# Kernel optimization log

Hardware: AMD Instinct MI355X
Metric: run time of the kernel (lower is better)

## Reference

```python
import jax, jax.numpy as jnp
import numpy as np

K = 1024          # num_embeddings
D = 64            # embedding_dim
EPS = 0.05        # entropic regularization epsilon
DUAL_STEPS = 10
DUAL_LR = 0.5
TEMP = 0.5        # hist_temperature
OT_W = 1.0
CC = 0.25         # commitment cost


def _norm_prob(p):
    p = jnp.clip(p, 1e-12)
    return p / p.sum()


def _dual_obj(phi, src_w, tgt_w, cost):
    src_w = _norm_prob(src_w)
    tgt_w = _norm_prob(tgt_w)
    log_tgt = jnp.log(jnp.clip(tgt_w, 1e-12))[None, :]          # [1, K]
    lse = jax.scipy.special.logsumexp(log_tgt + (-cost + phi[None, :]) / EPS, axis=1)  # [K]
    return jnp.sum(src_w * (-EPS * lse)) + jnp.sum(tgt_w * phi)


def _dual_ot_loss(src_w, tgt_w, cost):
    src_d = jax.lax.stop_gradient(src_w)
    tgt_d = jax.lax.stop_gradient(tgt_w)
    cost_d = jax.lax.stop_gradient(cost)
    grad_phi = jax.grad(_dual_obj)
    def body(_, phi):
        return phi + DUAL_LR * grad_phi(phi, src_d, tgt_d, cost_d)
    phi = jax.lax.fori_loop(0, DUAL_STEPS, body, jnp.zeros_like(tgt_d))
    return _dual_obj(jax.lax.stop_gradient(phi), src_w, tgt_w, cost)


def _gaussian_target():
    idx = jnp.arange(K, dtype=jnp.float32)
    mean = (K - 1) / 2.0
    std = K / 6.0
    t = jnp.exp(-0.5 * ((idx - mean) / std) ** 2)
    return t / jnp.clip(t.sum(), 1e-12)


def _forward(inputs, codebook):
    B, C, H, W = inputs.shape
    x_bhwc = jnp.transpose(inputs, (0, 2, 3, 1))                 # [B,H,W,C]
    flat = x_bhwc.reshape(-1, C)                                  # [N, D]
    # squared-distance matrix [N, K]
    d = (jnp.sum(flat * flat, axis=1, keepdims=True)
         + jnp.sum(codebook * codebook, axis=1)
         - 2.0 * flat @ codebook.T)
    idx = jnp.argmin(d, axis=1)                                   # [N]
    enc = jax.nn.one_hot(idx, K, dtype=jnp.float32)               # [N, K]
    # power normalize (one-hot power = sqrt(1/K) < 1, so a no-op, but faithful)
    power = jnp.sqrt(jnp.mean(enc * enc))
    enc = jnp.where(power > 1.0, enc / power, enc)
    clean_q = enc @ codebook                                      # [N, D]
    noisy_q = clean_q                                             # channel=None -> zero noise
    # training losses
    hard_hist = jnp.mean(enc, axis=0)                             # [K]
    soft = jax.nn.softmax(-d / TEMP, axis=1)                      # [N, K]
    soft_hist = jnp.mean(soft, axis=0)
    # value = hard_hist, gradient flows via soft_hist (straight-through hist)
    cw = _norm_prob(hard_hist + soft_hist - jax.lax.stop_gradient(soft_hist))
    target = _gaussian_target()
    support = jnp.arange(K, dtype=jnp.float32)
    cost = jnp.abs(support[:, None] - support[None, :])           # cdist(p=2) on 1-d support
    ot_loss = OT_W * _dual_ot_loss(cw, target, cost)
    codebook_loss = jnp.mean((clean_q - jax.lax.stop_gradient(flat)) ** 2)
    commit_loss = jnp.mean((jax.lax.stop_gradient(clean_q) - flat) ** 2)
    loss = codebook_loss + CC * commit_loss + ot_loss
    # straight-through quantized output
    nq = noisy_q.reshape(B, H, W, C)
    quantized = x_bhwc + jax.lax.stop_gradient(nq - x_bhwc)
    quantized = jnp.transpose(quantized, (0, 3, 1, 2))            # [B,C,H,W]
    avg = jnp.mean(enc, axis=0)
    perplexity = jnp.exp(-jnp.sum(avg * jnp.log(avg + 1e-10)))
    return quantized, loss, perplexity


def setup_inputs() -> dict:
    key = jax.random.key(0)
    k1, k2 = jax.random.split(key)
    inputs = jax.random.normal(k1, (32, D, 32, 32), dtype=jnp.float32)
    codebook = jax.random.uniform(k2, (K, D), minval=-1.0 / K, maxval=1.0 / K, dtype=jnp.float32)
    return {"inputs": inputs, "codebook": codebook}


def reference(inputs, codebook):
    return _forward(inputs, codebook)
```

## Files before the change

### kernel.cpp

```cpp
#include <hip/hip_runtime.h>
#include <math.h>

#define NPTS 32768
#define KCB  1024
#define DIM  64
#define HW   1024
#define CHW  65536
#define RWIN 2

typedef short  bf16x8 __attribute__((ext_vector_type(8)));
typedef float  f32x16 __attribute__((ext_vector_type(16)));

__device__ __forceinline__ unsigned short f2b_rne(float f) {
  unsigned u = __float_as_uint(f);
  unsigned r = 0x7FFFu + ((u >> 16) & 1u);
  return (unsigned short)((u + r) >> 16);
}

__device__ __forceinline__ float block_sum(float v, float* scratch) {
  #pragma unroll
  for (int o = 32; o > 0; o >>= 1) v += __shfl_down(v, o, 64);
  int wid  = threadIdx.x >> 6;
  int lane = threadIdx.x & 63;
  __syncthreads();
  if (lane == 0) scratch[wid] = v;
  __syncthreads();
  float s = 0.f;
  int nw = blockDim.x >> 6;
  for (int w = 0; w < nw; ++w) s += scratch[w];
  return s;
}

__global__ __launch_bounds__(64) void k_cvt(const float* __restrict__ cb,
                                            float4* __restrict__ cbf,
                                            float* __restrict__ cnorm) {
  int c = blockIdx.x * 64 + threadIdx.x;
  const float4* row4 = (const float4*)(cb + c * DIM);
  float4 r[16];
  #pragma unroll
  for (int i = 0; i < 16; ++i) r[i] = row4[i];
  float s = 0.f;
  #pragma unroll
  for (int i = 0; i < 16; ++i) {
    s = fmaf(r[i].x, r[i].x, s); s = fmaf(r[i].y, r[i].y, s);
    s = fmaf(r[i].z, r[i].z, s); s = fmaf(r[i].w, r[i].w, s);
  }
  cnorm[c] = s;
  int ch = c >> 6, nt = (c >> 5) & 1, n = c & 31;
  int base = ch * 1024 + nt * 256 + n;
  #pragma unroll
  for (int o = 0; o < 8; ++o) {
    float f[8] = {r[2*o].x, r[2*o].y, r[2*o].z, r[2*o].w,
                  r[2*o+1].x, r[2*o+1].y, r[2*o+1].z, r[2*o+1].w};
    unsigned hu[4], lu[4];
    #pragma unroll
    for (int j = 0; j < 4; ++j) {
      unsigned short h0 = f2b_rne(f[2*j]),   h1 = f2b_rne(f[2*j+1]);
      float hf0 = __uint_as_float((unsigned)h0 << 16);
      float hf1 = __uint_as_float((unsigned)h1 << 16);
      unsigned short l0 = f2b_rne(f[2*j] - hf0), l1 = f2b_rne(f[2*j+1] - hf1);
      hu[j] = (unsigned)h0 | ((unsigned)h1 << 16);
      lu[j] = (unsigned)l0 | ((unsigned)l1 << 16);
    }
    int pos = base + (o >> 1) * 64 + (o & 1) * 32;
    uint4 hv = {hu[0], hu[1], hu[2], hu[3]};
    uint4 lv = {lu[0], lu[1], lu[2], lu[3]};
    cbf[pos]       = *(float4*)&hv;
    cbf[pos + 512] = *(float4*)&lv;
  }
}

__global__ __launch_bounds__(256, 2) void k_dist(const float* __restrict__ x,
                                                 const float* __restrict__ cb,
                                                 const float4* __restrict__ cbf,
                                                 const float* __restrict__ cnorm,
                                                 int* __restrict__ hist,
                                                 float* __restrict__ msep,
                                                 float* __restrict__ out) {
  __shared__ unsigned short lph[64][72], lpl[64][72];
  __shared__ short bbuf[2][8192];
  __shared__ float s_cn[KCB];
  __shared__ float s_sx[64], s_part[4][64];
  __shared__ unsigned long long s_pk[64][2];
  __shared__ int   s_bd[64];
  __shared__ float scratch[4];

  int tid = threadIdx.x;
  int t   = blockIdx.x;
  int n0  = t * 64;
  int b   = n0 >> 10;
  int hw0 = n0 & 1023;

  *(float4*)&s_cn[tid * 4] = *(const float4*)(cnorm + tid * 4);

  {
    int p = tid & 63, q4 = tid >> 6;
    const float* xb = x + b * CHW + hw0 + p;
    float s = 0.f;
    unsigned short hb[16], lb[16];
    #pragma unroll
    for (int i = 0; i < 16; ++i) {
      int c = q4 * 16 + i;
      float f = xb[c * HW];
      s = fmaf(f, f, s);
      unsigned short h = f2b_rne(f);
      float hf = __uint_as_float(((unsigned)h) << 16);
      hb[i] = h;
      lb[i] = f2b_rne(f - hf);
    }
    s_part[q4][p] = s;
    #pragma unroll
    for (int j = 0; j < 8; ++j) {
      *(unsigned*)&lph[p][q4 * 16 + 2 * j] = (unsigned)hb[2*j] | ((unsigned)hb[2*j+1] << 16);
      *(unsigned*)&lpl[p][q4 * 16 + 2 * j] = (unsigned)lb[2*j] | ((unsigned)lb[2*j+1] << 16);
    }
  }
  float4 pf[4];
  #pragma unroll
  for (int j = 0; j < 4; ++j) pf[j] = cbf[tid + 256 * j];
  __syncthreads();
  if (tid < 64)
    s_sx[tid] = ((s_part[0][tid] + s_part[1][tid]) + s_part[2][tid]) + s_part[3][tid];
  __syncthreads();

  int w = tid >> 6, l = tid & 63;
  int wm = w >> 1, wn = w & 1;
  int u = l >> 5, n = l & 31;

  bf16x8 ah[4], al[4];
  {
    int pt = wm * 32 + n;
    #pragma unroll
    for (int s = 0; s < 4; ++s) {
      ah[s] = *(const bf16x8*)&lph[pt][(2 * s + u) * 8];
      al[s] = *(const bf16x8*)&lpl[pt][(2 * s + u) * 8];
    }
  }
  float sxr[16];
  #pragma unroll
  for (int r = 0; r < 16; ++r)
    sxr[r] = s_sx[wm * 32 + (r & 3) + 8 * (r >> 2) + 4 * u];

  float best[16]; int bidx[16];
  #pragma unroll
  for (int r = 0; r < 16; ++r) { best[r] = 3.4e38f; bidx[r] = 0; }

  int bofs = wn * 256 + u * 32 + n;

  for (int ch = 0; ch < 16; ++ch) {
    int bb = ch & 1;
    #pragma unroll
    for (int j = 0; j < 4; ++j)
      *(float4*)&bbuf[bb][(tid + 256 * j) * 8] = pf[j];
    if (ch < 15) {
      #pragma unroll
      for (int j = 0; j < 4; ++j)
        pf[j] = cbf[(ch + 1) * 1024 + tid + 256 * j];
    }
    __builtin_amdgcn_s_waitcnt(0xc07f);
    __builtin_amdgcn_s_barrier();

    f32x16 acc;
    #pragma unroll
    for (int r = 0; r < 16; ++r) acc[r] = 0.f;
    #pragma unroll
    for (int s = 0; s < 4; ++s) {
      bf16x8 bh = *(const bf16x8*)&bbuf[bb][(bofs + s * 64) * 8];
      bf16x8 bl = *(const bf16x8*)&bbuf[bb][(bofs + s * 64 + 512) * 8];
      acc = __builtin_amdgcn_mfma_f32_32x32x16_bf16(ah[s], bh, acc, 0, 0, 0);
      acc = __builtin_amdgcn_mfma_f32_32x32x16_bf16(ah[s], bl, acc, 0, 0, 0);
      acc = __builtin_amdgcn_mfma_f32_32x32x16_bf16(al[s], bh, acc, 0, 0, 0);
    }
    float cnv = s_cn[ch * 64 + wn * 32 + n];
    int   kk  = ch * 64 + wn * 32 + n;
    #pragma unroll
    for (int r = 0; r < 16; ++r) {
      float dist = (sxr[r] + cnv) - 2.0f * acc[r];
      if (dist < best[r]) { best[r] = dist; bidx[r] = kk; }
    }
  }

  #pragma unroll
  for (int r = 0; r < 16; ++r) {
    unsigned long long p =
        ((unsigned long long)__float_as_uint(best[r]) << 32) | (unsigned)bidx[r];
    #pragma unroll
    for (int m = 1; m < 32; m <<= 1) {
      unsigned long long o = __shfl_xor(p, m, 64);
      p = (o < p) ? o : p;
    }
    if (n == 0)
      s_pk[wm * 32 + (r & 3) + 8 * (r >> 2) + 4 * u][wn] = p;
  }
  __syncthreads();
  if (tid < 64) {
    unsigned long long a = s_pk[tid][0], c2 = s_pk[tid][1];
    unsigned long long mn = (c2 < a) ? c2 : a;
    int bd = (int)(mn & 0xffffffffull);
    s_bd[tid] = bd;
    atomicAdd(&hist[bd], 1);
  }
  __syncthreads();

  float se = 0.f;
  {
    int p = tid & 63, cg = tid >> 6;
    int bd = s_bd[p];
    const float* crow = cb + bd * DIM;
    const float* xp = x + b * CHW + hw0 + p;
    float* ob = out + b * CHW + hw0 + p;
    #pragma unroll 4
    for (int i = 0; i < 16; ++i) {
      int c = cg * 16 + i;
      float xv   = xp[c * HW];
      float diff = crow[c] - xv;
      se += diff * diff;
      ob[c * HW] = xv + diff;
    }
  }
  float tot = block_sum(se, scratch);
  if (tid == 0) msep[t] = tot;
}

__global__ __launch_bounds__(256) void k_ot(const int* __restrict__ hist,
                                            const float* __restrict__ msep,
                                            float* __restrict__ out) {
  __shared__ __align__(16) float s_lt[KCB + 8], s_src[KCB + 8],
                                 s_phi[KCB + 8], s_lse[KCB + 8];
  __shared__ float scratch[4];
  int tid = threadIdx.x;
  int i0  = tid * 4;
  int sl0 = i0 + 4;

  float msetot = block_sum(msep[tid] + msep[tid + 256], scratch);

  int4 hi4 = *(const int4*)(hist + i0);
  int  hi[4] = {hi4.x, hi4.y, hi4.z, hi4.w};
  float tj[4], hj[4];
  #pragma unroll
  for (int j = 0; j < 4; ++j) {
    float fi = (float)(i0 + j);
    float zz = (fi - 511.5f) / (1024.0f / 6.0f);
    tj[j] = expf(-0.5f * zz * zz);
    hj[j] = (float)hi[j] * (1.0f / 32768.0f);
  }
  float St = block_sum(tj[0] + tj[1] + tj[2] + tj[3], scratch);
  float tgt[4], ltw[4];
  float l2 = 0.f;
  #pragma unroll
  for (int j = 0; j < 4; ++j) { tgt[j] = fmaxf(tj[j] / fmaxf(St, 1e-12f), 1e-12f); l2 += tgt[j]; }
  float St2 = block_sum(l2, scratch);
  #pragma unroll
  for (int j = 0; j < 4; ++j) { tgt[j] = tgt[j] / St2; ltw[j] = logf(fmaxf(tgt[j], 1e-12f)); }

  float m1[4], srcw[4];
  float l3 = 0.f;
  #pragma unroll
  for (int j = 0; j < 4; ++j) { m1[j] = fmaxf(hj[j], 1e-12f); l3 += m1[j]; }
  float S1 = block_sum(l3, scratch);
  float l4 = 0.f;
  #pragma unroll
  for (int j = 0; j < 4; ++j) { srcw[j] = fmaxf(m1[j] / S1, 1e-12f); l4 += srcw[j]; }
  float S2 = block_sum(l4, scratch);
  float l5 = 0.f;
  #pragma unroll
  for (int j = 0; j < 4; ++j) { srcw[j] = srcw[j] / S2; l5 += hj[j] * logf(hj[j] + 1e-10f); }
  float ent = block_sum(l5, scratch);

  *(float4*)&s_lt[sl0]  = *(float4*)ltw;
  *(float4*)&s_src[sl0] = *(float4*)srcw;
  *(float4*)&s_phi[sl0] = make_float4(0.f, 0.f, 0.f, 0.f);
  *(float4*)&s_lse[sl0] = make_float4(0.f, 0.f, 0.f, 0.f);
  if (tid == 0) {
    #pragma unroll
    for (int p = 0; p < 4; ++p) {
      s_lt[p] = -100.f; s_src[p] = 0.f; s_phi[p] = 0.f; s_lse[p] = 0.f;
      s_lt[KCB+4+p] = -100.f; s_src[KCB+4+p] = 0.f; s_phi[KCB+4+p] = 0.f; s_lse[KCB+4+p] = 0.f;
    }
  }
  __syncthreads();

  float ws[12];
  #pragma unroll
  for (int m = 0; m < 3; ++m) *(float4*)&ws[m*4] = *(float4*)&s_src[i0 + m*4];

  float phi[4] = {0.f, 0.f, 0.f, 0.f};
  float lse[4];
  for (int it = 0; it <= 10; ++it) {
    float wl[12], wp[12];
    #pragma unroll
    for (int m = 0; m < 3; ++m) {
      *(float4*)&wl[m*4] = *(float4*)&s_lt[i0 + m*4];
      *(float4*)&wp[m*4] = *(float4*)&s_phi[i0 + m*4];
    }
    #pragma unroll
    for (int j = 0; j < 4; ++j) {
      float mx = -3.0e38f;
      float vv[5];
      #pragma unroll
      for (int qq = 0; qq < 5; ++qq) {
        int m = j + qq + 2;
        float a = wl[m] + (wp[m] - fabsf((float)(qq - 2))) * 20.0f;
        vv[qq] = a;
        mx = fmaxf(mx, a);
      }
      float ssum = 0.f;
      #pragma unroll
      for (int qq = 0; qq < 5; ++qq) ssum += expf(vv[qq] - mx);
      lse[j] = mx + logf(ssum);
    }
    *(float4*)&s_lse[sl0] = *(float4*)lse;
    __syncthreads();
    if (it == 10) break;

    float we[12];
    #pragma unroll
    for (int m = 0; m < 3; ++m) *(float4*)&we[m*4] = *(float4*)&s_lse[i0 + m*4];
    #pragma unroll
    for (int j = 0; j < 4; ++j) {
      float basej = ltw[j] + phi[j] * 20.0f;
      float cs = 0.f;
      #pragma unroll
      for (int qq = 0; qq < 5; ++qq) {
        int m = j + qq + 2;
        float a = basej - fabsf((float)(qq - 2)) * 20.0f;
        cs += ws[m] * expf(a - we[m]);
      }
      phi[j] += 0.5f * (tgt[j] - cs);
    }
    *(float4*)&s_phi[sl0] = *(float4*)phi;
    __syncthreads();
  }

  float lo = 0.f;
  #pragma unroll
  for (int j = 0; j < 4; ++j) lo += srcw[j] * (-0.05f * lse[j]) + tgt[j] * phi[j];
  float ot = block_sum(lo, scratch);

  if (tid == 0) {
    out[2097152] = 1.25f * (msetot * (1.0f / 2097152.0f)) + ot;
    out[2097153] = expf(-ent);
  }
}

extern "C" void kernel_launch(void* const* d_in, const int* in_sizes, int n_in,
                              void* d_out, int out_size, void* d_ws, size_t ws_size,
                              hipStream_t stream) {
  const float* x  = (const float*)d_in[0];
  const float* cb = (const float*)d_in[1];
  float* out = (float*)d_out;

  float4* cbf  = (float4*)d_ws;
  float*  cnorm = (float*)((char*)d_ws + 262144);
  int*    hist  = (int*)((char*)d_ws + 266240);
  float*  msep  = (float*)((char*)d_ws + 270336);

  hipMemsetAsync(hist, 0, 4096, stream);
  k_cvt<<<16, 64, 0, stream>>>(cb, cbf, cnorm);
  k_dist<<<512, 256, 0, stream>>>(x, cb, cbf, cnorm, hist, msep, out);
  k_ot<<<1, 256, 0, stream>>>(hist, msep, out);
}
```

Measured before the change: 130.4 us.

## Split codebook search across two wave halves, reuse x registers, fold hist memset

Doubles the distance-kernel block to 512 threads. Each half of the block scans half of the codebook chunks against the same 64 points, and the per-row argmin is then merged across four partial results in shared memory. The input values loaded for the bf16 split are kept in registers and reused for the straight-through output, which avoids a second global read of x. The histogram memset is folded into the codebook conversion kernel, removing one launch. The trade-off is more threads per block, a shared-memory region reused between the A tiles and the B buffers, and extra barriers per chunk.

```diff
diff --git a/kernel.cpp b/kernel.cpp
--- a/kernel.cpp
+++ b/kernel.cpp
@@ -6,7 +6,6 @@
 #define DIM  64
 #define HW   1024
 #define CHW  65536
-#define RWIN 2
 
 typedef short  bf16x8 __attribute__((ext_vector_type(8)));
 typedef float  f32x16 __attribute__((ext_vector_type(16)));
@@ -33,8 +32,10 @@
 
 __global__ __launch_bounds__(64) void k_cvt(const float* __restrict__ cb,
                                             float4* __restrict__ cbf,
-                                            float* __restrict__ cnorm) {
+                                            float* __restrict__ cnorm,
+                                            int* __restrict__ hist) {
   int c = blockIdx.x * 64 + threadIdx.x;
+  hist[c] = 0;
   const float4* row4 = (const float4*)(cb + c * DIM);
   float4 r[16];
   #pragma unroll
@@ -70,20 +71,22 @@
   }
 }
 
-__global__ __launch_bounds__(256, 2) void k_dist(const float* __restrict__ x,
+__global__ __launch_bounds__(512, 4) void k_dist(const float* __restrict__ x,
                                                  const float* __restrict__ cb,
                                                  const float4* __restrict__ cbf,
                                                  const float* __restrict__ cnorm,
                                                  int* __restrict__ hist,
                                                  float* __restrict__ msep,
                                                  float* __restrict__ out) {
-  __shared__ unsigned short lph[64][72], lpl[64][72];
-  __shared__ short bbuf[2][8192];
+  __shared__ __align__(16) short s_big[16384];
   __shared__ float s_cn[KCB];
   __shared__ float s_sx[64], s_part[4][64];
-  __shared__ unsigned long long s_pk[64][2];
+  __shared__ unsigned long long s_pk[64][4];
   __shared__ int   s_bd[64];
-  __shared__ float scratch[4];
+  __shared__ float scratch[8];
+
+  unsigned short (*lph)[72] = (unsigned short (*)[72])&s_big[0];
+  unsigned short (*lpl)[72] = (unsigned short (*)[72])&s_big[4608];
 
   int tid = threadIdx.x;
   int t   = blockIdx.x;
@@ -91,9 +94,15 @@
   int b   = n0 >> 10;
   int hw0 = n0 & 1023;
 
-  *(float4*)&s_cn[tid * 4] = *(const float4*)(cnorm + tid * 4);
-
-  {
+  int hh = tid >> 8, r2 = tid & 255;
+
+  float4 pf[4];
+  #pragma unroll
+  for (int j = 0; j < 4; ++j) pf[j] = cbf[hh * 8192 + r2 + 256 * j];
+
+  float fx[16];
+  if (tid < 256) {
+    *(float4*)&s_cn[tid * 4] = *(const float4*)(cnorm + tid * 4);
     int p = tid & 63, q4 = tid >> 6;
     const float* xb = x + b * CHW + hw0 + p;
     float s = 0.f;
@@ -102,10 +111,11 @@
     for (int i = 0; i < 16; ++i) {
       int c = q4 * 16 + i;
       float f = xb[c * HW];
+      fx[i] = f;
       s = fmaf(f, f, s);
-      unsigned short h = f2b_rne(f);
-      float hf = __uint_as_float(((unsigned)h) << 16);
-      hb[i] = h;
+      unsigned short hsh = f2b_rne(f);
+      float hf = __uint_as_float(((unsigned)hsh) << 16);
+      hb[i] = hsh;
       lb[i] = f2b_rne(f - hf);
     }
     s_part[q4][p] = s;
@@ -115,16 +125,15 @@
       *(unsigned*)&lpl[p][q4 * 16 + 2 * j] = (unsigned)lb[2*j] | ((unsigned)lb[2*j+1] << 16);
     }
   }
-  float4 pf[4];
-  #pragma unroll
-  for (int j = 0; j < 4; ++j) pf[j] = cbf[tid + 256 * j];
-  __syncthreads();
+  __builtin_amdgcn_s_waitcnt(0xc07f);
+  __builtin_amdgcn_s_barrier();
   if (tid < 64)
     s_sx[tid] = ((s_part[0][tid] + s_part[1][tid]) + s_part[2][tid]) + s_part[3][tid];
-  __syncthreads();
+  __builtin_amdgcn_s_waitcnt(0xc07f);
+  __builtin_amdgcn_s_barrier();
 
   int w = tid >> 6, l = tid & 63;
-  int wm = w >> 1, wn = w & 1;
+  int h = w >> 2, wm = (w >> 1) & 1, wn = w & 1;
   int u = l >> 5, n = l & 31;
 
   bf16x8 ah[4], al[4];
@@ -146,33 +155,38 @@
   for (int r = 0; r < 16; ++r) { best[r] = 3.4e38f; bidx[r] = 0; }
 
   int bofs = wn * 256 + u * 32 + n;
-
-  for (int ch = 0; ch < 16; ++ch) {
-    int bb = ch & 1;
+  const short* bbr = &s_big[h  * 8192];
+  short*       bbw = &s_big[hh * 8192];
+
+  for (int i = 0; i < 8; ++i) {
+    __builtin_amdgcn_s_waitcnt(0xc07f);
+    __builtin_amdgcn_s_barrier();
+    __builtin_amdgcn_sched_barrier(0);
     #pragma unroll
     for (int j = 0; j < 4; ++j)
-      *(float4*)&bbuf[bb][(tid + 256 * j) * 8] = pf[j];
-    if (ch < 15) {
+      *(float4*)&bbw[(r2 + 256 * j) * 8] = pf[j];
+    if (i < 7) {
       #pragma unroll
       for (int j = 0; j < 4; ++j)
-        pf[j] = cbf[(ch + 1) * 1024 + tid + 256 * j];
+        pf[j] = cbf[(hh * 8 + i + 1) * 1024 + r2 + 256 * j];
     }
     __builtin_amdgcn_s_waitcnt(0xc07f);
     __builtin_amdgcn_s_barrier();
+    __builtin_amdgcn_sched_barrier(0);
 
     f32x16 acc;
     #pragma unroll
     for (int r = 0; r < 16; ++r) acc[r] = 0.f;
     #pragma unroll
     for (int s = 0; s < 4; ++s) {
-      bf16x8 bh = *(const bf16x8*)&bbuf[bb][(bofs + s * 64) * 8];
-      bf16x8 bl = *(const bf16x8*)&bbuf[bb][(bofs + s * 64 + 512) * 8];
+      bf16x8 bh = *(const bf16x8*)&bbr[(bofs + s * 64) * 8];
+      bf16x8 bl = *(const bf16x8*)&bbr[(bofs + s * 64 + 512) * 8];
       acc = __builtin_amdgcn_mfma_f32_32x32x16_bf16(ah[s], bh, acc, 0, 0, 0);
       acc = __builtin_amdgcn_mfma_f32_32x32x16_bf16(ah[s], bl, acc, 0, 0, 0);
       acc = __builtin_amdgcn_mfma_f32_32x32x16_bf16(al[s], bh, acc, 0, 0, 0);
     }
-    float cnv = s_cn[ch * 64 + wn * 32 + n];
-    int   kk  = ch * 64 + wn * 32 + n;
+    int   kk  = (h * 8 + i) * 64 + wn * 32 + n;
+    float cnv = s_cn[kk];
     #pragma unroll
     for (int r = 0; r < 16; ++r) {
       float dist = (sxr[r] + cnv) - 2.0f * acc[r];
@@ -190,11 +204,14 @@
       p = (o < p) ? o : p;
     }
     if (n == 0)
-      s_pk[wm * 32 + (r & 3) + 8 * (r >> 2) + 4 * u][wn] = p;
+      s_pk[wm * 32 + (r & 3) + 8 * (r >> 2) + 4 * u][h * 2 + wn] = p;
   }
   __syncthreads();
   if (tid < 64) {
-    unsigned long long a = s_pk[tid][0], c2 = s_pk[tid][1];
+    unsigned long long m0 = s_pk[tid][0], m1 = s_pk[tid][1];
+    unsigned long long m2 = s_pk[tid][2], m3 = s_pk[tid][3];
+    unsigned long long a  = (m1 < m0) ? m1 : m0;
+    unsigned long long c2 = (m3 < m2) ? m3 : m2;
     unsigned long long mn = (c2 < a) ? c2 : a;
     int bd = (int)(mn & 0xffffffffull);
     s_bd[tid] = bd;
@@ -203,16 +220,15 @@
   __syncthreads();
 
   float se = 0.f;
-  {
+  if (tid < 256) {
     int p = tid & 63, cg = tid >> 6;
     int bd = s_bd[p];
     const float* crow = cb + bd * DIM;
-    const float* xp = x + b * CHW + hw0 + p;
     float* ob = out + b * CHW + hw0 + p;
     #pragma unroll 4
     for (int i = 0; i < 16; ++i) {
       int c = cg * 16 + i;
-      float xv   = xp[c * HW];
+      float xv   = fx[i];
       float diff = crow[c] - xv;
       se += diff * diff;
       ob[c * HW] = xv + diff;
@@ -355,8 +371,7 @@
   int*    hist  = (int*)((char*)d_ws + 266240);
   float*  msep  = (float*)((char*)d_ws + 270336);
 
-  hipMemsetAsync(hist, 0, 4096, stream);
-  k_cvt<<<16, 64, 0, stream>>>(cb, cbf, cnorm);
-  k_dist<<<512, 256, 0, stream>>>(x, cb, cbf, cnorm, hist, msep, out);
+  k_cvt<<<16, 64, 0, stream>>>(cb, cbf, cnorm, hist);
+  k_dist<<<512, 512, 0, stream>>>(x, cb, cbf, cnorm, hist, msep, out);
   k_ot<<<1, 256, 0, stream>>>(hist, msep, out);
 }
```

Result: slower. 145.7 us (+11.7%).

## Load codebook MFMA operands directly from global into registers, drop LDS staging

Applied to the files above, without the earlier changes.

The distance kernel now reads the pre-swizzled bf16 codebook fragments straight from global memory into registers, with a one-chunk register prefetch. This replaces the LDS double-buffer and per-chunk barriers, and the chunk loop is fully unrolled. The input values are kept in registers to avoid re-reading x in the epilogue, and the histogram memset is folded into the conversion kernel to remove one launch. Each wave now issues redundant global/L2 loads of the codebook and uses more registers, which may reduce occupancy.

```diff
diff --git a/kernel.cpp b/kernel.cpp
--- a/kernel.cpp
+++ b/kernel.cpp
@@ -6,7 +6,6 @@
 #define DIM  64
 #define HW   1024
 #define CHW  65536
-#define RWIN 2
 
 typedef short  bf16x8 __attribute__((ext_vector_type(8)));
 typedef float  f32x16 __attribute__((ext_vector_type(16)));
@@ -33,8 +32,10 @@
 
 __global__ __launch_bounds__(64) void k_cvt(const float* __restrict__ cb,
                                             float4* __restrict__ cbf,
-                                            float* __restrict__ cnorm) {
+                                            float* __restrict__ cnorm,
+                                            int* __restrict__ hist) {
   int c = blockIdx.x * 64 + threadIdx.x;
+  hist[c] = 0;
   const float4* row4 = (const float4*)(cb + c * DIM);
   float4 r[16];
   #pragma unroll
@@ -78,7 +79,6 @@
                                                  float* __restrict__ msep,
                                                  float* __restrict__ out) {
   __shared__ unsigned short lph[64][72], lpl[64][72];
-  __shared__ short bbuf[2][8192];
   __shared__ float s_cn[KCB];
   __shared__ float s_sx[64], s_part[4][64];
   __shared__ unsigned long long s_pk[64][2];
@@ -93,6 +93,7 @@
 
   *(float4*)&s_cn[tid * 4] = *(const float4*)(cnorm + tid * 4);
 
+  float fx[16];
   {
     int p = tid & 63, q4 = tid >> 6;
     const float* xb = x + b * CHW + hw0 + p;
@@ -102,6 +103,7 @@
     for (int i = 0; i < 16; ++i) {
       int c = q4 * 16 + i;
       float f = xb[c * HW];
+      fx[i] = f;
       s = fmaf(f, f, s);
       unsigned short h = f2b_rne(f);
       float hf = __uint_as_float(((unsigned)h) << 16);
@@ -115,9 +117,6 @@
       *(unsigned*)&lpl[p][q4 * 16 + 2 * j] = (unsigned)lb[2*j] | ((unsigned)lb[2*j+1] << 16);
     }
   }
-  float4 pf[4];
-  #pragma unroll
-  for (int j = 0; j < 4; ++j) pf[j] = cbf[tid + 256 * j];
   __syncthreads();
   if (tid < 64)
     s_sx[tid] = ((s_part[0][tid] + s_part[1][tid]) + s_part[2][tid]) + s_part[3][tid];
@@ -146,37 +145,44 @@
   for (int r = 0; r < 16; ++r) { best[r] = 3.4e38f; bidx[r] = 0; }
 
   int bofs = wn * 256 + u * 32 + n;
-
+  const bf16x8* gb = (const bf16x8*)cbf;
+
+  bf16x8 cbh[4], cbl[4], nbh[4], nbl[4];
+  #pragma unroll
+  for (int s = 0; s < 4; ++s) {
+    cbh[s] = gb[bofs + s * 64];
+    cbl[s] = gb[bofs + s * 64 + 512];
+  }
+
+  #pragma unroll
   for (int ch = 0; ch < 16; ++ch) {
-    int bb = ch & 1;
-    #pragma unroll
-    for (int j = 0; j < 4; ++j)
-      *(float4*)&bbuf[bb][(tid + 256 * j) * 8] = pf[j];
     if (ch < 15) {
-      #pragma unroll
-      for (int j = 0; j < 4; ++j)
-        pf[j] = cbf[(ch + 1) * 1024 + tid + 256 * j];
-    }
-    __builtin_amdgcn_s_waitcnt(0xc07f);
-    __builtin_amdgcn_s_barrier();
-
+      const bf16x8* gn = gb + (ch + 1) * 1024;
+      #pragma unroll
+      for (int s = 0; s < 4; ++s) {
+        nbh[s] = gn[bofs + s * 64];
+        nbl[s] = gn[bofs + s * 64 + 512];
+      }
+    }
     f32x16 acc;
     #pragma unroll
     for (int r = 0; r < 16; ++r) acc[r] = 0.f;
     #pragma unroll
     for (int s = 0; s < 4; ++s) {
-      bf16x8 bh = *(const bf16x8*)&bbuf[bb][(bofs + s * 64) * 8];
-      bf16x8 bl = *(const bf16x8*)&bbuf[bb][(bofs + s * 64 + 512) * 8];
-      acc = __builtin_amdgcn_mfma_f32_32x32x16_bf16(ah[s], bh, acc, 0, 0, 0);
-      acc = __builtin_amdgcn_mfma_f32_32x32x16_bf16(ah[s], bl, acc, 0, 0, 0);
-      acc = __builtin_amdgcn_mfma_f32_32x32x16_bf16(al[s], bh, acc, 0, 0, 0);
-    }
-    float cnv = s_cn[ch * 64 + wn * 32 + n];
+      acc = __builtin_amdgcn_mfma_f32_32x32x16_bf16(ah[s], cbh[s], acc, 0, 0, 0);
+      acc = __builtin_amdgcn_mfma_f32_32x32x16_bf16(ah[s], cbl[s], acc, 0, 0, 0);
+      acc = __builtin_amdgcn_mfma_f32_32x32x16_bf16(al[s], cbh[s], acc, 0, 0, 0);
+    }
     int   kk  = ch * 64 + wn * 32 + n;
+    float cnv = s_cn[kk];
     #pragma unroll
     for (int r = 0; r < 16; ++r) {
       float dist = (sxr[r] + cnv) - 2.0f * acc[r];
       if (dist < best[r]) { best[r] = dist; bidx[r] = kk; }
+    }
+    if (ch < 15) {
+      #pragma unroll
+      for (int s = 0; s < 4; ++s) { cbh[s] = nbh[s]; cbl[s] = nbl[s]; }
     }
   }
 
@@ -207,12 +213,11 @@
     int p = tid & 63, cg = tid >> 6;
     int bd = s_bd[p];
     const float* crow = cb + bd * DIM;
-    const float* xp = x + b * CHW + hw0 + p;
     float* ob = out + b * CHW + hw0 + p;
     #pragma unroll 4
     for (int i = 0; i < 16; ++i) {
       int c = cg * 16 + i;
-      float xv   = xp[c * HW];
+      float xv   = fx[i];
       float diff = crow[c] - xv;
       se += diff * diff;
       ob[c * HW] = xv + diff;
@@ -355,8 +360,7 @@
   int*    hist  = (int*)((char*)d_ws + 266240);
   float*  msep  = (float*)((char*)d_ws + 270336);
 
-  hipMemsetAsync(hist, 0, 4096, stream);
-  k_cvt<<<16, 64, 0, stream>>>(cb, cbf, cnorm);
+  k_cvt<<<16, 64, 0, stream>>>(cb, cbf, cnorm, hist);
   k_dist<<<512, 256, 0, stream>>>(x, cb, cbf, cnorm, hist, msep, out);
   k_ot<<<1, 256, 0, stream>>>(hist, msep, out);
 }
```

Measured after the change: 109.0 us. 1.2x faster.
